# Kernel optimization log

Measured on AMD Instinct MI355X. Metric: run time of the kernel, lower is better.

Reference implementation:

```python
import jax, jax.numpy as jnp
import numpy as np

B, N, F_IN, F_OUT = 16, 1024, 128, 128

def setup_inputs() -> dict:
    key = jax.random.key(0)
    k1, k2, k3 = jax.random.split(key, 3)
    X = jax.random.normal(k1, (B, N, F_IN), dtype=jnp.float32)
    A = jax.random.uniform(k2, (B, N, N), dtype=jnp.float32)
    W = jax.random.normal(k3, (F_IN, F_OUT), dtype=jnp.float32)
    return {"X": X, "A": A, "W": W}

def reference(X, A, W):
    # A_hat = A + I  (batched add of identity)
    n = A.shape[-1]
    A_hat = A + jnp.eye(n, dtype=A.dtype)  # [B,N,N]
    # D_hat^{-1/2} applied as elementwise row/col scaling (torch builds diag
    # matrices and inverts; mathematically identical for diagonal D).
    deg = jnp.sum(A_hat, axis=-1)               # [B,N]
    d_inv_sqrt = 1.0 / jnp.sqrt(deg)            # [B,N]
    A_norm = A_hat * d_inv_sqrt[:, :, None] * d_inv_sqrt[:, None, :]  # [B,N,N]
    out = jnp.einsum('bnm,bmf->bnf', A_norm, X)  # aggregation bmm
    out = jnp.einsum('bnf,fg->bng', out, W)      # weight matmul
    return out
```

## Files before the change

kernel.cpp:

```cpp
#include <hip/hip_runtime.h>

#define NN 1024
#define FF 128

typedef __attribute__((ext_vector_type(8))) short bf16x8;
typedef __attribute__((ext_vector_type(4))) float f32x4;

__device__ __forceinline__ unsigned short f2bf(float x) {
  unsigned u = __float_as_uint(x);
  u += 0x7fff + ((u >> 16) & 1);
  return (unsigned short)(u >> 16);
}
__device__ __forceinline__ float bf2f(unsigned short b) {
  return __uint_as_float(((unsigned)b) << 16);
}
__device__ __forceinline__ bf16x8 cvt8(float4 a, float4 b) {
  bf16x8 r;
  r[0] = (short)f2bf(a.x); r[1] = (short)f2bf(a.y);
  r[2] = (short)f2bf(a.z); r[3] = (short)f2bf(a.w);
  r[4] = (short)f2bf(b.x); r[5] = (short)f2bf(b.y);
  r[6] = (short)f2bf(b.z); r[7] = (short)f2bf(b.w);
  return r;
}

__device__ __forceinline__ void gl_lds16(const void* g, void* l) {
  __builtin_amdgcn_global_load_lds(
      (const __attribute__((address_space(1))) unsigned*)g,
      (__attribute__((address_space(3))) unsigned*)l, 16, 0, 0);
}

__global__ __launch_bounds__(256) void k_degxw(const float* __restrict__ A,
                                               const float* __restrict__ X,
                                               const float* __restrict__ W,
                                               float* __restrict__ d,
                                               unsigned short* __restrict__ Yt) {
  if (blockIdx.x >= 256) {
    int row  = (blockIdx.x - 256) * 4 + (threadIdx.x >> 6);
    int lane = threadIdx.x & 63;
    const float4* Ar = (const float4*)(A + (size_t)row * NN);
    float s = 0.f;
#pragma unroll
    for (int i = 0; i < 4; ++i) {
      float4 v = Ar[lane + i * 64];
      s += (v.x + v.y) + (v.z + v.w);
    }
#pragma unroll
    for (int off = 32; off > 0; off >>= 1) s += __shfl_down(s, off, 64);
    if (lane == 0) d[row] = rsqrtf(s + 1.0f);
    return;
  }

  __shared__ __align__(16) unsigned short Xs[64 * 128];
  __shared__ __align__(16) unsigned short Ws[128 * 128];
  int t  = threadIdx.x;
  int b  = blockIdx.x >> 4;
  int m0 = (blockIdx.x & 15) * 64;

#pragma unroll
  for (int j = 0; j < 4; ++j) {
    int id = t + j * 256;
    int r = id >> 4, p = id & 15, c = p ^ (r & 15);
    const float* gp = X + ((size_t)(b * NN + m0 + r) * FF + c * 8);
    float4 v0 = *(const float4*)gp;
    float4 v1 = *(const float4*)(gp + 4);
    *(bf16x8*)&Xs[r * 128 + p * 8] = cvt8(v0, v1);
  }
  {
    int f = t >> 1, gh = (t & 1) * 64;
    const float* wrow = W + (size_t)f * FF + gh;
    int c8 = (f >> 3);
    int e  = f & 7;
#pragma unroll
    for (int j4 = 0; j4 < 16; ++j4) {
      float4 wv = *(const float4*)(wrow + j4 * 4);
#pragma unroll
      for (int k = 0; k < 4; ++k) {
        int g = gh + j4 * 4 + k;
        float v = (k == 0) ? wv.x : (k == 1) ? wv.y : (k == 2) ? wv.z : wv.w;
        Ws[g * 128 + ((c8 ^ (g & 15)) * 8) + e] = f2bf(v);
      }
    }
  }
  __syncthreads();

  int wave = t >> 6, lane = t & 63, quad = lane >> 4, l16 = lane & 15;
  f32x4 acc[8];
#pragma unroll
  for (int ct = 0; ct < 8; ++ct) acc[ct] = (f32x4){0.f, 0.f, 0.f, 0.f};

#pragma unroll
  for (int ks = 0; ks < 4; ++ks) {
    int q = ks * 4 + quad;
    bf16x8 a = *(const bf16x8*)&Xs[(wave * 16 + l16) * 128 + (q ^ l16) * 8];
#pragma unroll
    for (int ct = 0; ct < 8; ++ct) {
      bf16x8 w = *(const bf16x8*)&Ws[(ct * 16 + l16) * 128 + (q ^ l16) * 8];
      acc[ct] = __builtin_amdgcn_mfma_f32_16x16x32_bf16(a, w, acc[ct], 0, 0, 0);
    }
  }

  int mb = wave * 16 + quad * 4;
#pragma unroll
  for (int ct = 0; ct < 8; ++ct) {
    int g = ct * 16 + l16;
    ushort4 p;
    p.x = f2bf(acc[ct][0]);
    p.y = f2bf(acc[ct][1]);
    p.z = f2bf(acc[ct][2]);
    p.w = f2bf(acc[ct][3]);
    *(ushort4*)(Yt + (size_t)(b * 128 + g) * NN + m0 + mb) = p;
  }
}

__global__ __launch_bounds__(256) void k_agg(const float* __restrict__ A,
                                             const unsigned short* __restrict__ Yt,
                                             const float* __restrict__ d,
                                             float* __restrict__ out) {
  __shared__ __align__(16) float          Asf[3][32 * 64];
  __shared__ __align__(16) unsigned short Ys[3][128 * 64];
  __shared__ __align__(16) float          dl[NN];
  int t   = threadIdx.x;
  int bid = blockIdx.x;
  int xcd = bid & 7;
  int j   = bid >> 3;
  int b   = xcd + 8 * (j >> 5);
  int n0  = (j & 31) * 32;
  int wave = t >> 6, lane = t & 63, quad = lane >> 4, l16 = lane & 15;
  int wr = wave >> 1, wc = wave & 1;

  const float*          Ab = A  + (size_t)(b * NN + n0) * NN;
  const unsigned short* Yb = Yt + (size_t)b * 128 * NN;

  *(float4*)&dl[t * 4] = *(const float4*)(d + (size_t)b * NN + t * 4);
  __syncthreads();

  int ra = lane >> 4, pa_s = lane & 15;
  int ry_s = lane >> 3, py_s = lane & 7;

  auto issue = [&](int k0, int bufi) {
#pragma unroll
    for (int jj = 0; jj < 2; ++jj) {
      int r = wave * 8 + jj * 4 + ra;
      int c = pa_s ^ (2 * (r & 7));
      gl_lds16(Ab + ((size_t)r * NN + k0 + c * 4), &Asf[bufi][(wave * 8 + jj * 4) * 64]);
    }
#pragma unroll
    for (int jj = 0; jj < 4; ++jj) {
      int ry = wave * 32 + jj * 8 + ry_s;
      int c  = py_s ^ (ry & 7);
      gl_lds16(Yb + ((size_t)ry * NN + k0 + c * 8), &Ys[bufi][(wave * 32 + jj * 8) * 64]);
    }
  };

  f32x4 acc[4];
#pragma unroll
  for (int ct = 0; ct < 4; ++ct) acc[ct] = (f32x4){0.f, 0.f, 0.f, 0.f};

  int swA = 2 * (l16 & 7);
  issue(0, 0);
  issue(64, 1);

#pragma unroll
  for (int s = 0; s < 16; ++s) {
    if (s < 15) asm volatile("s_waitcnt vmcnt(6)" ::: "memory");
    else        asm volatile("s_waitcnt vmcnt(0)" ::: "memory");
    __builtin_amdgcn_s_barrier();
    const float*          as = &Asf[s % 3][0];
    const unsigned short* ys = &Ys[s % 3][0];
    int k0 = s * 64;
    __builtin_amdgcn_s_setprio(1);
#pragma unroll
    for (int ks = 0; ks < 2; ++ks) {
      int cq = ks * 4 + quad;
      int pa = (2 * cq) ^ swA;
      float4 a0 = *(const float4*)&as[(wr * 16 + l16) * 64 + pa * 4];
      float4 a1 = *(const float4*)&as[(wr * 16 + l16) * 64 + pa * 4 + 4];
      float4 dv0 = *(const float4*)&dl[k0 + cq * 8];
      float4 dv1 = *(const float4*)&dl[k0 + cq * 8 + 4];
      a0.x *= dv0.x; a0.y *= dv0.y; a0.z *= dv0.z; a0.w *= dv0.w;
      a1.x *= dv1.x; a1.y *= dv1.y; a1.z *= dv1.z; a1.w *= dv1.w;
      bf16x8 a = cvt8(a0, a1);
#pragma unroll
      for (int ct = 0; ct < 4; ++ct) {
        int cp = (cq ^ (l16 & 7)) * 8;
        bf16x8 y = *(const bf16x8*)&ys[(wc * 64 + ct * 16 + l16) * 64 + cp];
        acc[ct] = __builtin_amdgcn_mfma_f32_16x16x32_bf16(a, y, acc[ct], 0, 0, 0);
      }
    }
    __builtin_amdgcn_s_setprio(0);
    __builtin_amdgcn_sched_barrier(0);
    if (s < 14) issue((s + 2) * 64, (s + 2) % 3);
  }

  int nb = n0 + wr * 16 + quad * 4;
  float4 d4 = *(const float4*)&dl[nb];
#pragma unroll
  for (int ct = 0; ct < 4; ++ct) {
    int g = wc * 64 + ct * 16 + l16;
    ushort4 yv = *(const ushort4*)(Yt + (size_t)(b * 128 + g) * NN + nb);
    float* op = out + ((size_t)(b * NN + nb) * FF + g);
    op[0 * FF] = d4.x * (acc[ct][0] + d4.x * bf2f(yv.x));
    op[1 * FF] = d4.y * (acc[ct][1] + d4.y * bf2f(yv.y));
    op[2 * FF] = d4.z * (acc[ct][2] + d4.z * bf2f(yv.z));
    op[3 * FF] = d4.w * (acc[ct][3] + d4.w * bf2f(yv.w));
  }
}

extern "C" void kernel_launch(void* const* d_in, const int* in_sizes, int n_in,
                              void* d_out, int out_size, void* d_ws, size_t ws_size,
                              hipStream_t stream) {
  const float* X = (const float*)d_in[0];
  const float* A = (const float*)d_in[1];
  const float* W = (const float*)d_in[2];
  float* out = (float*)d_out;

  char* ws = (char*)d_ws;
  float*          dinv = (float*)ws;
  unsigned short* Yt   = (unsigned short*)(ws + 65536);

  k_degxw<<<dim3(256 + 4096), dim3(256), 0, stream>>>(A, X, W, dinv, Yt);
  k_agg  <<<dim3(512),        dim3(256), 0, stream>>>(A, Yt, dinv, out);
}
```

Before: 117.6 us.

## Split aggregation output columns across two blocks and double-buffer loads

The aggregation kernel now assigns each block half of the 128 output features, doubling the grid to 1024 blocks for more parallelism across CUs. The pipeline goes from triple to double buffering with a smaller LDS footprint and launch bounds that request four blocks per CU. In exchange, the A tile (the dominant traffic) is now read twice, once per feature half, and an extra barrier per iteration is added.

```diff
diff --git a/kernel.cpp b/kernel.cpp
--- a/kernel.cpp
+++ b/kernel.cpp
@@ -112,24 +112,26 @@
   }
 }
 
-__global__ __launch_bounds__(256) void k_agg(const float* __restrict__ A,
-                                             const unsigned short* __restrict__ Yt,
-                                             const float* __restrict__ d,
-                                             float* __restrict__ out) {
-  __shared__ __align__(16) float          Asf[3][32 * 64];
-  __shared__ __align__(16) unsigned short Ys[3][128 * 64];
+__global__ __launch_bounds__(256, 4) void k_agg(const float* __restrict__ A,
+                                                const unsigned short* __restrict__ Yt,
+                                                const float* __restrict__ d,
+                                                float* __restrict__ out) {
+  __shared__ __align__(16) float          Asf[2][32 * 64];
+  __shared__ __align__(16) unsigned short Ys[2][64 * 64];
   __shared__ __align__(16) float          dl[NN];
   int t   = threadIdx.x;
   int bid = blockIdx.x;
   int xcd = bid & 7;
   int j   = bid >> 3;
-  int b   = xcd + 8 * (j >> 5);
-  int n0  = (j & 31) * 32;
+  int b   = xcd + 8 * (j >> 6);
+  int sub = j & 63;
+  int n0  = (sub & 31) * 32;
+  int gh  = (sub >> 5) * 64;
   int wave = t >> 6, lane = t & 63, quad = lane >> 4, l16 = lane & 15;
   int wr = wave >> 1, wc = wave & 1;
 
   const float*          Ab = A  + (size_t)(b * NN + n0) * NN;
-  const unsigned short* Yb = Yt + (size_t)b * 128 * NN;
+  const unsigned short* Yb = Yt + ((size_t)(b * 128 + gh)) * NN;
 
   *(float4*)&dl[t * 4] = *(const float4*)(d + (size_t)b * NN + t * 4);
   __syncthreads();
@@ -142,31 +144,36 @@
     for (int jj = 0; jj < 2; ++jj) {
       int r = wave * 8 + jj * 4 + ra;
       int c = pa_s ^ (2 * (r & 7));
-      gl_lds16(Ab + ((size_t)r * NN + k0 + c * 4), &Asf[bufi][(wave * 8 + jj * 4) * 64]);
-    }
-#pragma unroll
-    for (int jj = 0; jj < 4; ++jj) {
-      int ry = wave * 32 + jj * 8 + ry_s;
+      gl_lds16(Ab + ((size_t)r * NN + k0 + c * 4),
+               &Asf[bufi][(wave * 8 + jj * 4) * 64]);
+    }
+#pragma unroll
+    for (int jj = 0; jj < 2; ++jj) {
+      int ry = wave * 16 + jj * 8 + ry_s;
       int c  = py_s ^ (ry & 7);
-      gl_lds16(Yb + ((size_t)ry * NN + k0 + c * 8), &Ys[bufi][(wave * 32 + jj * 8) * 64]);
+      gl_lds16(Yb + ((size_t)ry * NN + k0 + c * 8),
+               &Ys[bufi][(wave * 16 + jj * 8) * 64]);
     }
   };
 
-  f32x4 acc[4];
-#pragma unroll
-  for (int ct = 0; ct < 4; ++ct) acc[ct] = (f32x4){0.f, 0.f, 0.f, 0.f};
+  f32x4 acc[2];
+  acc[0] = (f32x4){0.f, 0.f, 0.f, 0.f};
+  acc[1] = (f32x4){0.f, 0.f, 0.f, 0.f};
 
   int swA = 2 * (l16 & 7);
   issue(0, 0);
-  issue(64, 1);
 
 #pragma unroll
   for (int s = 0; s < 16; ++s) {
-    if (s < 15) asm volatile("s_waitcnt vmcnt(6)" ::: "memory");
-    else        asm volatile("s_waitcnt vmcnt(0)" ::: "memory");
+    if (s < 15) {
+      issue((s + 1) * 64, (s + 1) & 1);
+      asm volatile("s_waitcnt vmcnt(4)" ::: "memory");
+    } else {
+      asm volatile("s_waitcnt vmcnt(0)" ::: "memory");
+    }
     __builtin_amdgcn_s_barrier();
-    const float*          as = &Asf[s % 3][0];
-    const unsigned short* ys = &Ys[s % 3][0];
+    const float*          as = &Asf[s & 1][0];
+    const unsigned short* ys = &Ys[s & 1][0];
     int k0 = s * 64;
     __builtin_amdgcn_s_setprio(1);
 #pragma unroll
@@ -181,22 +188,22 @@
       a1.x *= dv1.x; a1.y *= dv1.y; a1.z *= dv1.z; a1.w *= dv1.w;
       bf16x8 a = cvt8(a0, a1);
 #pragma unroll
-      for (int ct = 0; ct < 4; ++ct) {
+      for (int ct = 0; ct < 2; ++ct) {
         int cp = (cq ^ (l16 & 7)) * 8;
-        bf16x8 y = *(const bf16x8*)&ys[(wc * 64 + ct * 16 + l16) * 64 + cp];
+        bf16x8 y = *(const bf16x8*)&ys[(wc * 32 + ct * 16 + l16) * 64 + cp];
         acc[ct] = __builtin_amdgcn_mfma_f32_16x16x32_bf16(a, y, acc[ct], 0, 0, 0);
       }
     }
     __builtin_amdgcn_s_setprio(0);
     __builtin_amdgcn_sched_barrier(0);
-    if (s < 14) issue((s + 2) * 64, (s + 2) % 3);
+    __builtin_amdgcn_s_barrier();
   }
 
   int nb = n0 + wr * 16 + quad * 4;
   float4 d4 = *(const float4*)&dl[nb];
 #pragma unroll
-  for (int ct = 0; ct < 4; ++ct) {
-    int g = wc * 64 + ct * 16 + l16;
+  for (int ct = 0; ct < 2; ++ct) {
+    int g = gh + wc * 32 + ct * 16 + l16;
     ushort4 yv = *(const ushort4*)(Yt + (size_t)(b * 128 + g) * NN + nb);
     float* op = out + ((size_t)(b * NN + nb) * FF + g);
     op[0 * FF] = d4.x * (acc[ct][0] + d4.x * bf2f(yv.x));
@@ -219,5 +226,5 @@
   unsigned short* Yt   = (unsigned short*)(ws + 65536);
 
   k_degxw<<<dim3(256 + 4096), dim3(256), 0, stream>>>(A, X, W, dinv, Yt);
-  k_agg  <<<dim3(512),        dim3(256), 0, stream>>>(A, Yt, dinv, out);
-}
+  k_agg  <<<dim3(1024),       dim3(256), 0, stream>>>(A, Yt, dinv, out);
+}
```

Measured after the change: 120.9 us. 1.03x slower.
